# Kernel tuning notes

Measured on AMD Instinct MI355X. Metric: run time of the kernel, lower is better.

The kernel has to match this reference:

```python
import jax, jax.numpy as jnp
import numpy as np

POOLED = 7      # kernel_size
SCALE = 0.25    # spatial_scale
GMAX = 2        # upper bound of adaptive sampling grid (box sizes chosen so ceil(roi/7) <= 2)


def setup_inputs() -> dict:
    key = jax.random.key(0)
    k1, k2, k3, k4, k5, k6 = jax.random.split(key, 6)
    B, C, H, W, K = 4, 256, 128, 128, 1000
    features = jax.random.normal(k1, (B, C, H, W), dtype=jnp.float32)
    img = H / SCALE  # 512.0: image-space extent
    bidx = jax.random.randint(k2, (K,), 0, B).astype(jnp.float32)
    bw = jax.random.uniform(k3, (K,), minval=8.0, maxval=56.0)
    bh = jax.random.uniform(k4, (K,), minval=8.0, maxval=56.0)
    x1 = jax.random.uniform(k5, (K,), minval=0.0, maxval=img - 56.0)
    y1 = jax.random.uniform(k6, (K,), minval=0.0, maxval=img - 56.0)
    boxes = jnp.stack([bidx, x1, y1, x1 + bw, y1 + bh], axis=1)
    return {"features": features, "boxes": boxes}


def _sample_coords(start, bin_sz, grid):
    # start/bin_sz/grid: [K] -> coords [K, POOLED, GMAX]
    p = jnp.arange(POOLED, dtype=jnp.float32)
    i = jnp.arange(GMAX, dtype=jnp.float32)
    return (start[:, None, None] + p[None, :, None] * bin_sz[:, None, None]
            + (i[None, None, :] + 0.5) * bin_sz[:, None, None] / grid[:, None, None])


def roi_align(features, boxes):
    B, C, H, W = features.shape
    K = boxes.shape[0]
    b = boxes[:, 0].astype(jnp.int32)
    x1, y1, x2, y2 = (boxes[:, i] * SCALE for i in (1, 2, 3, 4))
    # aligned=False: no -0.5 offset, clamp roi size to >= 1
    roi_w = jnp.maximum(x2 - x1, 1.0)
    roi_h = jnp.maximum(y2 - y1, 1.0)
    bin_w = roi_w / POOLED
    bin_h = roi_h / POOLED
    # sampling_ratio = -1 -> adaptive grid = ceil(roi_size / pooled)
    gh = jnp.ceil(roi_h / POOLED)
    gw = jnp.ceil(roi_w / POOLED)

    y = _sample_coords(y1, bin_h, gh)  # [K,7,GMAX]
    x = _sample_coords(x1, bin_w, gw)  # [K,7,GMAX]
    vy = (jnp.arange(GMAX)[None, None, :] < gh[:, None, None])  # [K,1,GMAX]
    vx = (jnp.arange(GMAX)[None, None, :] < gw[:, None, None])

    # full sample grid [K, 7, GMAX, 7, GMAX] -> flatten to [K, P]
    shp = (K, POOLED, GMAX, POOLED, GMAX)
    Y = jnp.broadcast_to(y[:, :, :, None, None], shp).reshape(K, -1)
    X = jnp.broadcast_to(x[:, None, None, :, :], shp).reshape(K, -1)
    V = jnp.broadcast_to(vy[:, :, :, None, None] & vx[:, None, None, :, :], shp).reshape(K, -1)

    # bilinear interpolation, torchvision boundary semantics
    inval = (Y < -1.0) | (Y > H) | (X < -1.0) | (X > W)
    Yc = jnp.clip(Y, 0.0)
    Xc = jnp.clip(X, 0.0)
    yl = jnp.minimum(Yc.astype(jnp.int32), H - 1)
    xl = jnp.minimum(Xc.astype(jnp.int32), W - 1)
    yh = jnp.minimum(yl + 1, H - 1)
    xh = jnp.minimum(xl + 1, W - 1)
    Yc = jnp.where(yl >= H - 1, yl.astype(jnp.float32), Yc)
    Xc = jnp.where(xl >= W - 1, xl.astype(jnp.float32), Xc)
    ly = Yc - yl
    lx = Xc - xl
    hy = 1.0 - ly
    hx = 1.0 - lx
    m = jnp.where(inval | (~V), 0.0, 1.0)
    w1 = hy * hx * m; w2 = hy * lx * m; w3 = ly * hx * m; w4 = ly * lx * m

    def gather(yi, xi):
        # advanced indexing: [K,P] indices -> [K,P,C]
        return features[b[:, None], :, yi, xi]

    val = (w1[..., None] * gather(yl, xl) + w2[..., None] * gather(yl, xh)
           + w3[..., None] * gather(yh, xl) + w4[..., None] * gather(yh, xh))  # [K,P,C]
    val = val.reshape(K, POOLED, GMAX, POOLED, GMAX, C)
    out = val.sum(axis=(2, 4)) / (gh * gw)[:, None, None, None]  # [K,7,7,C]
    return jnp.transpose(out, (0, 3, 1, 2))  # [K,C,7,7]


def reference(features, boxes):
    return roi_align(features, boxes)
```

## Files before the change

kernel.cpp:

```cpp
#include <hip/hip_runtime.h>

#define POOLED 7
#define SCALE  0.25f
#define CCH    256
#define HH     128
#define WW     128
#define HW     (HH * WW)

#define NCH      16
#define NCHUNK   2
#define NBLK_PER_BOX (CCH / (NCH * NCHUNK))
#define PATCH_H  15
#define NV       5
#define PIXROW   19
#define NPIX     (PATCH_H * PIXROW)
#define CHPAD    20
#define ROWSTR   (PIXROW * CHPAD)

__global__ __launch_bounds__(256) void roi_align_kernel(
    const float* __restrict__ feat,
    const float* __restrict__ boxes,
    float* __restrict__ out,
    int K)
{
    __shared__ __align__(16) float patch[NPIX * CHPAD];

    int bx = blockIdx.x;
    int k  = bx >> 3;
    int cb = (bx & 7) * (NCH * NCHUNK);
    if (k >= K) return;
    int t = threadIdx.x;

    const float* box = boxes + k * 5;
    int   b  = (int)box[0];
    float x1 = box[1] * SCALE;
    float y1 = box[2] * SCALE;
    float x2 = box[3] * SCALE;
    float y2 = box[4] * SCALE;

    float roi_w = fmaxf(x2 - x1, 1.0f);
    float roi_h = fmaxf(y2 - y1, 1.0f);
    float bin_w = roi_w * (1.0f / POOLED);
    float bin_h = roi_h * (1.0f / POOLED);
    int gw = (int)ceilf(roi_w * (1.0f / POOLED));
    int gh = (int)ceilf(roi_h * (1.0f / POOLED));
    float inv_gh = 1.0f / (float)gh;
    float inv_gw = 1.0f / (float)gw;

    float ymin = y1 + 0.5f * bin_h * inv_gh;
    float ymax = y1 + 6 * bin_h + ((gh - 1) + 0.5f) * bin_h * inv_gh;
    float xmin = x1 + 0.5f * bin_w * inv_gw;

    int ylo = min((int)fmaxf(ymin, 0.0f), HH - 1);
    int xlo = min((int)fmaxf(xmin, 0.0f), WW - 1);
    int xlo4 = xlo & ~3;
    int ylmax = min((int)fmaxf(ymax, 0.0f), HH - 1);
    int h_p = min(ylmax + 1, HH - 1) - ylo + 1;
    if (h_p > PATCH_H) h_p = PATCH_H;
    int mcr = min(WW - 1 - xlo4, (xlo - xlo4) + 14);

    int s_b   = __builtin_amdgcn_readfirstlane(b);
    int s_ylo = __builtin_amdgcn_readfirstlane(ylo);
    int s_x4  = __builtin_amdgcn_readfirstlane(xlo4);
    int s_hp  = __builtin_amdgcn_readfirstlane(h_p);
    int s_mcr = __builtin_amdgcn_readfirstlane(mcr);
    int s_ns  = __builtin_amdgcn_readfirstlane(gh * gw);
    int ghm   = __builtin_amdgcn_readfirstlane(gh - 1);

    int p  = t & 63;
    int pc = min(p, 48);
    int pw = pc % POOLED;
    int ph = pc / POOLED;
    int cg = t >> 6;

    float yb = y1 + ph * bin_h;
    float xb = x1 + pw * bin_w;

    float hy0, ly0, hy1, ly1;
    int   ryT0, ryhT0, ryT1, ryhT1;
    float hx0, lx0, hx1, lx1;
    int   rxT0, rxhT0, rxT1, rxhT1;

#define YSIDE(IYC, HY, LY, RT, RHT) {                                   \
        float y = yb + IYC * bin_h * inv_gh;                            \
        bool vld = (y >= -1.0f) && (y <= (float)HH);                    \
        float yc = fmaxf(y, 0.0f);                                      \
        int yl = min((int)yc, HH - 1);                                  \
        int yh2 = min(yl + 1, HH - 1);                                  \
        float ly = (yl >= HH - 1) ? 0.0f : (yc - (float)yl);            \
        HY = vld ? (1.0f - ly) : 0.0f;                                  \
        LY = vld ? ly : 0.0f;                                           \
        int ry  = max(0, min(yl  - s_ylo, s_hp - 1));                   \
        int ryh = max(0, min(yh2 - s_ylo, s_hp - 1));                   \
        RT  = ry  * ROWSTR;                                             \
        RHT = ryh * ROWSTR;                                             \
    }
#define XSIDE(IXC, HX, LX, RT, RHT) {                                   \
        float x = xb + IXC * bin_w * inv_gw;                            \
        bool vld = (x >= -1.0f) && (x <= (float)WW);                    \
        float xc = fmaxf(x, 0.0f);                                      \
        int xl = min((int)xc, WW - 1);                                  \
        int xh2 = min(xl + 1, WW - 1);                                  \
        float lx = (xl >= WW - 1) ? 0.0f : (xc - (float)xl);            \
        HX = vld ? (1.0f - lx) : 0.0f;                                  \
        LX = vld ? lx : 0.0f;                                           \
        int rxl = max(0, min(xl  - s_x4, PIXROW - 1));                  \
        int rxh = max(0, min(xh2 - s_x4, PIXROW - 1));                  \
        RT  = rxl * CHPAD;                                              \
        RHT = rxh * CHPAD;                                              \
    }
    YSIDE(0.5f, hy0, ly0, ryT0, ryhT0)
    YSIDE(1.5f, hy1, ly1, ryT1, ryhT1)
    XSIDE(0.5f, hx0, lx0, rxT0, rxhT0)
    XSIDE(1.5f, hx1, lx1, rxT1, rxhT1)
#undef YSIDE
#undef XSIDE

    float wa[4], wb[4], wc_[4], wd[4];
    int   oa[4], ob[4], oc[4], od[4];
    wa[0] = hy0 * hx0; wb[0] = hy0 * lx0; wc_[0] = ly0 * hx0; wd[0] = ly0 * lx0;
    oa[0] = ryT0 + rxT0;  ob[0] = ryT0 + rxhT0;
    oc[0] = ryhT0 + rxT0; od[0] = ryhT0 + rxhT0;
    {
        float hyS = ghm ? hy1 : hy0, lyS = ghm ? ly1 : ly0;
        int ryS = ghm ? ryT1 : ryT0, ryhS = ghm ? ryhT1 : ryhT0;
        float hxS = ghm ? hx0 : hx1, lxS = ghm ? lx0 : lx1;
        int rxS = ghm ? rxT0 : rxT1, rxhS = ghm ? rxhT0 : rxhT1;
        wa[1] = hyS * hxS; wb[1] = hyS * lxS; wc_[1] = lyS * hxS; wd[1] = lyS * lxS;
        oa[1] = ryS + rxS;  ob[1] = ryS + rxhS;
        oc[1] = ryhS + rxS; od[1] = ryhS + rxhS;
    }
    wa[2] = hy0 * hx1; wb[2] = hy0 * lx1; wc_[2] = ly0 * hx1; wd[2] = ly0 * lx1;
    oa[2] = ryT0 + rxT1;  ob[2] = ryT0 + rxhT1;
    oc[2] = ryhT0 + rxT1; od[2] = ryhT0 + rxhT1;
    wa[3] = hy1 * hx1; wb[3] = hy1 * lx1; wc_[3] = ly1 * hx1; wd[3] = ly1 * lx1;
    oa[3] = ryT1 + rxT1;  ob[3] = ryT1 + rxhT1;
    oc[3] = ryhT1 + rxT1; od[3] = ryhT1 + rxhT1;

    int lch = t >> 4;
    int sub = t & 15;
    int lim = s_hp * NV;
    const float* gch0 = feat + (s_b * CCH + cb + lch) * HW;

    bool act[NV], actw[NV];
    int  goff[NV];
    int  la[NV];
#pragma unroll
    for (int i = 0; i < NV; ++i) {
        int idx = i * 16 + sub;
        int r = idx / NV;
        int v = idx - r * NV;
        act[i]  = (idx < lim) && (4 * v <= s_mcr);
        actw[i] = act[i] && (v < 4);
        goff[i] = (s_ylo + r) * WW + min(s_x4 + 4 * v, WW - 4);
        la[i]   = (r * PIXROW + 4 * v) * CHPAD + lch;
    }

    float sc = inv_gh * inv_gw;

    float4 u0[NV];
#pragma unroll
    for (int i = 0; i < NV; ++i)
        if (act[i]) u0[i] = *(const float4*)(gch0 + goff[i]);
#pragma unroll
    for (int i = 0; i < NV; ++i)
        if (act[i]) {
            float* lp = patch + la[i];
            lp[0]         = u0[i].x;
            lp[CHPAD]     = u0[i].y;
            lp[2 * CHPAD] = u0[i].z;
            if (actw[i]) lp[3 * CHPAD] = u0[i].w;
        }

    const float* gch1 = gch0 + NCH * HW;
    float4 u1[NV];
#pragma unroll
    for (int i = 0; i < NV; ++i)
        if (act[i]) u1[i] = *(const float4*)(gch1 + goff[i]);

    __syncthreads();

#define BILIN(S) {                                                      \
        float4 va = *(const float4*)(cp + oa[S]);                       \
        float4 vb = *(const float4*)(cp + ob[S]);                       \
        float4 vc = *(const float4*)(cp + oc[S]);                       \
        float4 vd = *(const float4*)(cp + od[S]);                       \
        float w1 = wa[S], w2 = wb[S], w3 = wc_[S], w4 = wd[S];          \
        acc.x += w1 * va.x + w2 * vb.x + w3 * vc.x + w4 * vd.x;         \
        acc.y += w1 * va.y + w2 * vb.y + w3 * vc.y + w4 * vd.y;         \
        acc.z += w1 * va.z + w2 * vb.z + w3 * vc.z + w4 * vd.z;         \
        acc.w += w1 * va.w + w2 * vb.w + w3 * vc.w + w4 * vd.w;         \
    }
#define COMPUTE(CHB) {                                                  \
        float4 acc = {0.0f, 0.0f, 0.0f, 0.0f};                          \
        const float* cp = patch + cg * 4;                               \
        BILIN(0)                                                        \
        if (s_ns > 1) BILIN(1)                                          \
        if (s_ns > 2) { BILIN(2) BILIN(3) }                             \
        int ob_ = (k * CCH + cb + (CHB) + cg * 4) * 49 + p;             \
        out[ob_]          = acc.x * sc;                                 \
        out[ob_ + 49]     = acc.y * sc;                                 \
        out[ob_ + 2 * 49] = acc.z * sc;                                 \
        out[ob_ + 3 * 49] = acc.w * sc;                                 \
    }

    if (p < 49) COMPUTE(0)

    __syncthreads();

#pragma unroll
    for (int i = 0; i < NV; ++i)
        if (act[i]) {
            float* lp = patch + la[i];
            lp[0]         = u1[i].x;
            lp[CHPAD]     = u1[i].y;
            lp[2 * CHPAD] = u1[i].z;
            if (actw[i]) lp[3 * CHPAD] = u1[i].w;
        }
    __syncthreads();

    if (p < 49) COMPUTE(NCH)
}

extern "C" void kernel_launch(void* const* d_in, const int* in_sizes, int n_in,
                              void* d_out, int out_size, void* d_ws, size_t ws_size,
                              hipStream_t stream) {
    const float* feat  = (const float*)d_in[0];
    const float* boxes = (const float*)d_in[1];
    float* out = (float*)d_out;

    int K = in_sizes[1] / 5;
    int blocks = K * NBLK_PER_BOX;
    roi_align_kernel<<<blocks, 256, 0, stream>>>(feat, boxes, out, K);
}
```

Before: 128.5 us.

## Reorder boxes by batch and spatial quadrant to improve feature cache locality

Adds a single-block counting-sort kernel that buckets boxes by batch index and image quadrant, then writes a permutation into the workspace. The main kernel processes boxes in this permuted order, so that concurrently running blocks touch nearby feature regions and reuse L2/MALL-resident data. In exchange it adds a second kernel launch, a serial single-block pass over the boxes, and one indirect load per block. The sort is only used when a large enough workspace is provided.

Measured after the change: 128.0 us. About the same (-0.4%).

```diff
diff --git a/kernel.cpp b/kernel.cpp
--- a/kernel.cpp
+++ b/kernel.cpp
@@ -17,18 +17,51 @@
 #define CHPAD    20
 #define ROWSTR   (PIXROW * CHPAD)
 
+__global__ void box_sort_kernel(const float* __restrict__ boxes,
+                                int* __restrict__ perm, int K)
+{
+    __shared__ int hist[16];
+    __shared__ int base[16];
+    int t = threadIdx.x;
+    if (t < 16) hist[t] = 0;
+    __syncthreads();
+    for (int i = t; i < K; i += blockDim.x) {
+        const float* bp = boxes + i * 5;
+        int key = (((int)bp[0] & 3) << 2)
+                | ((bp[2] >= 256.0f) ? 2 : 0)
+                | ((bp[1] >= 256.0f) ? 1 : 0);
+        atomicAdd(&hist[key], 1);
+    }
+    __syncthreads();
+    if (t == 0) {
+        int acc = 0;
+        for (int j = 0; j < 16; ++j) { base[j] = acc; acc += hist[j]; }
+    }
+    __syncthreads();
+    for (int i = t; i < K; i += blockDim.x) {
+        const float* bp = boxes + i * 5;
+        int key = (((int)bp[0] & 3) << 2)
+                | ((bp[2] >= 256.0f) ? 2 : 0)
+                | ((bp[1] >= 256.0f) ? 1 : 0);
+        int pos = atomicAdd(&base[key], 1);
+        perm[pos] = i;
+    }
+}
+
 __global__ __launch_bounds__(256) void roi_align_kernel(
     const float* __restrict__ feat,
     const float* __restrict__ boxes,
     float* __restrict__ out,
+    const int* __restrict__ perm,
     int K)
 {
     __shared__ __align__(16) float patch[NPIX * CHPAD];
 
     int bx = blockIdx.x;
-    int k  = bx >> 3;
+    int kq = bx >> 3;
     int cb = (bx & 7) * (NCH * NCHUNK);
-    if (k >= K) return;
+    if (kq >= K) return;
+    int k = perm ? perm[kq] : kq;
     int t = threadIdx.x;
 
     const float* box = boxes + k * 5;
@@ -230,6 +263,11 @@
     float* out = (float*)d_out;
 
     int K = in_sizes[1] / 5;
+    int* perm = nullptr;
+    if (d_ws && ws_size >= (size_t)K * sizeof(int)) {
+        perm = (int*)d_ws;
+        box_sort_kernel<<<1, 1024, 0, stream>>>(boxes, perm, K);
+    }
     int blocks = K * NBLK_PER_BOX;
-    roi_align_kernel<<<blocks, 256, 0, stream>>>(feat, boxes, out, K);
+    roi_align_kernel<<<blocks, 256, 0, stream>>>(feat, boxes, out, perm, K);
 }
```
